# Performance work log

Hardware: AMD Instinct MI355X
Metric: run time of the kernel (lower is better)

## Reference

```python
import jax, jax.numpy as jnp
import numpy as np

WS = 8
NUM_HEADS = 8
BLUR_STRENGTH = 1.0
EPS = 1e-5


def setup_inputs() -> dict:
    key = jax.random.key(0)
    ks = jax.random.split(key, 8)
    B, C, H, W = 8, 256, 128, 128
    FF = 1024
    inp = {
        'x': jax.random.normal(ks[0], (B, C, H, W), jnp.float32),
        'blur_map': jax.random.uniform(ks[1], (B, 1, H // 4, W // 4), jnp.float32),
        'qkv_w': jax.random.normal(ks[2], (C, 3 * C), jnp.float32) * 0.02,
        'qkv_b': jnp.zeros((3 * C,), jnp.float32),
        'proj_w': jax.random.normal(ks[3], (C, C), jnp.float32) * 0.02,
        'proj_b': jnp.zeros((C,), jnp.float32),
        'ff1_w': jax.random.normal(ks[4], (C, FF), jnp.float32) * 0.02,
        'ff1_b': jnp.zeros((FF,), jnp.float32),
        'ff2_w': jax.random.normal(ks[5], (FF, C), jnp.float32) * 0.02,
        'ff2_b': jnp.zeros((C,), jnp.float32),
        'n1_g': jnp.ones((C,), jnp.float32),
        'n1_b': jnp.zeros((C,), jnp.float32),
        'n2_g': jnp.ones((C,), jnp.float32),
        'n2_b': jnp.zeros((C,), jnp.float32),
    }
    return inp


def _layer_norm(y, g, b):
    mu = jnp.mean(y, axis=-1, keepdims=True)
    var = jnp.mean(jnp.square(y - mu), axis=-1, keepdims=True)
    return (y - mu) * jax.lax.rsqrt(var + EPS) * g + b


def reference(x, blur_map, qkv_w, qkv_b, proj_w, proj_b, ff1_w, ff1_b, ff2_w, ff2_b, n1_g, n1_b, n2_g, n2_b):
    B, C, H, W = x.shape
    ws = WS
    h = NUM_HEADS
    hd = C // h
    T = ws * ws
    scale = C ** (-0.5)  # note: full dim, matching the torch module

    # window partition -> [nw, T, C]
    xw = x.reshape(B, C, H // ws, ws, W // ws, ws)
    xw = xw.transpose(0, 2, 4, 3, 5, 1).reshape(-1, T, C)
    nw = xw.shape[0]

    qkv = (xw @ qkv_w + qkv_b).reshape(nw, T, 3, h, hd).transpose(2, 0, 3, 1, 4)
    q, k, v = qkv[0], qkv[1], qkv[2]  # [nw, h, T, hd]

    attn = jnp.einsum('whid,whjd->whij', q, k) * scale

    # blur modulation along the key axis
    blur_down = jax.image.resize(blur_map, (B, 1, H, W), 'bilinear')
    blur_w = blur_down.reshape(B, 1, H // ws, ws, W // ws, ws)
    blur_w = blur_w.transpose(0, 2, 4, 3, 5, 1).reshape(nw, T)
    attn = attn * (1.0 + BLUR_STRENGTH * blur_w)[:, None, None, :]

    attn = jax.nn.softmax(attn, axis=-1)
    out = jnp.einsum('whij,whjd->whid', attn, v)
    out = out.transpose(0, 2, 1, 3).reshape(nw, T, C)
    out = out @ proj_w + proj_b

    x1 = xw + _layer_norm(out, n1_g, n1_b)
    ff = jnp.maximum(x1 @ ff1_w + ff1_b, 0.0) @ ff2_w + ff2_b
    x2 = x1 + _layer_norm(ff, n2_g, n2_b)

    # window reverse -> [B, C, H, W]
    x2 = x2.reshape(B, H // ws, W // ws, ws, ws, C)
    return x2.transpose(0, 5, 1, 3, 2, 4).reshape(B, C, H, W)
```

## Files before the change

kernel.cpp:

```cpp
#include <hip/hip_runtime.h>
#include <hip/hip_bf16.h>
#include <cstdint>

typedef _Float16 half8 __attribute__((ext_vector_type(8)));
typedef _Float16 half4 __attribute__((ext_vector_type(4)));
typedef float f32x4 __attribute__((ext_vector_type(4)));

__device__ __forceinline__ void gload_lds16(const _Float16* g, _Float16* l) {
  __builtin_amdgcn_global_load_lds(
      (const __attribute__((address_space(1))) void*)g,
      (__attribute__((address_space(3))) void*)l, 16, 0, 0);
}

#define KSWZ(r) ((((r) >> 1) & 3) << 3)

__global__ __launch_bounds__(256) void wtrans(const float* __restrict__ W,
                                              _Float16* __restrict__ WT, int K, int N) {
  int idx = blockIdx.x * 256 + threadIdx.x;
  if (idx >= K * N) return;
  int k = idx / N, n = idx - k * N;
  WT[(size_t)n * K + k] = (_Float16)W[idx];
}

__global__ __launch_bounds__(256) void blur_prep(const float* __restrict__ bm,
                                                 float* __restrict__ bw) {
  int idx = blockIdx.x * 256 + threadIdx.x;
  int wi = idx >> 6, t = idx & 63;
  int b = wi >> 8, wid = wi & 255;
  int hw = wid >> 4, ww = wid & 15;
  int hh = hw * 8 + (t >> 3), www = ww * 8 + (t & 7);
  float yf = (hh + 0.5f) * 0.25f - 0.5f;
  float xf = (www + 0.5f) * 0.25f - 0.5f;
  float yfl = floorf(yf), xfl = floorf(xf);
  float fy = yf - yfl, fx = xf - xfl;
  int y0 = (int)yfl, x0 = (int)xfl;
  int y1 = y0 + 1, x1 = x0 + 1;
  if (y0 < 0) y0 = 0; if (x0 < 0) x0 = 0;
  if (y1 > 31) y1 = 31; if (x1 > 31) x1 = 31;
  const float* p = bm + (size_t)b * 1024;
  float v00 = p[y0 * 32 + x0], v01 = p[y0 * 32 + x1];
  float v10 = p[y1 * 32 + x0], v11 = p[y1 * 32 + x1];
  float v0 = v00 + fx * (v01 - v00);
  float v1 = v10 + fx * (v11 - v10);
  bw[idx] = v0 + fy * (v1 - v0);
}

__global__ __launch_bounds__(256) void gather_x(const float* __restrict__ x,
                                                _Float16* __restrict__ xw) {
  const int c0 = blockIdx.x << 6;
  const int hh = blockIdx.y;
  const int b  = blockIdx.z;
  __shared__ float tile[64][133];
  const int tid = threadIdx.x;
  {
    const int cl = tid >> 7, p = tid & 127;
    const float* xp = x + ((size_t)(b * 256 + c0) * 128 + hh) * 128 + p;
#pragma unroll
    for (int i = 0; i < 32; ++i) {
      int c = i * 2 + cl;
      tile[c][p] = xp[(size_t)c * 16384];
    }
  }
  __syncthreads();
  const int w = tid >> 6, lane = tid & 63;
  const int hw = hh >> 3, ts = hh & 7;
#pragma unroll
  for (int i = 0; i < 32; ++i) {
    int pp = i * 4 + w;
    int row = ((b * 256 + hw * 16 + (pp >> 3)) << 6) + ts * 8 + (pp & 7);
    xw[(size_t)row * 256 + c0 + lane] = (_Float16)tile[lane][pp];
  }
}

__global__ __launch_bounds__(256) void scatter_out(const _Float16* __restrict__ x2,
                                                   float* __restrict__ out) {
  const int c0 = blockIdx.x << 6;
  const int hh = blockIdx.y;
  const int b  = blockIdx.z;
  __shared__ float tile[64][133];
  const int tid = threadIdx.x;
  const int w = tid >> 6, lane = tid & 63;
  const int hw = hh >> 3, ts = hh & 7;
#pragma unroll
  for (int i = 0; i < 32; ++i) {
    int pp = i * 4 + w;
    int row = ((b * 256 + hw * 16 + (pp >> 3)) << 6) + ts * 8 + (pp & 7);
    tile[lane][pp] = (float)x2[(size_t)row * 256 + c0 + lane];
  }
  __syncthreads();
  const int cl = tid >> 7, p = tid & 127;
  float* op = out + ((size_t)(b * 256 + c0) * 128 + hh) * 128 + p;
#pragma unroll
  for (int i = 0; i < 32; ++i) {
    int c = i * 2 + cl;
    op[(size_t)c * 16384] = tile[c][p];
  }
}

template<int RELU>
__global__ __launch_bounds__(256) void gemm_f16(const _Float16* __restrict__ A,
    const _Float16* __restrict__ BT, const float* __restrict__ bias,
    _Float16* __restrict__ C, int M, int N, int K) {
  __shared__ _Float16 As[2][128 * 32];
  __shared__ _Float16 Bs[2][128 * 32];
  const int tid = threadIdx.x;
  const int gx = gridDim.x;
  int flat = blockIdx.y * gx + blockIdx.x;
  int nwg = gx * gridDim.y;
  int nb = (nwg & 7) ? flat : ((flat & 7) * (nwg >> 3) + (flat >> 3));
  const int m0 = (nb / gx) << 7;
  const int n0 = (nb % gx) << 7;
  const int w = tid >> 6, lane = tid & 63;
  const int wr = (w >> 1) << 6, wc = (w & 1) << 6;
  const int lr = lane & 15, lg = lane >> 4;
  f32x4 acc[4][4] = {};
  const int sr = tid >> 2, skk = ((tid & 3) << 3) ^ KSWZ(tid >> 2);
  const _Float16* Ag = A + (size_t)(m0 + sr) * K + skk;
  const _Float16* Bg = BT + (size_t)(n0 + sr) * K + skk;
  const size_t halfstep = (size_t)64 * K;
#define GSTAGE(bufi, k0) do { \
    gload_lds16(Ag + (k0),            &As[bufi][(size_t)tid * 8]); \
    gload_lds16(Ag + (k0) + halfstep, &As[bufi][(size_t)(256 + tid) * 8]); \
    gload_lds16(Bg + (k0),            &Bs[bufi][(size_t)tid * 8]); \
    gload_lds16(Bg + (k0) + halfstep, &Bs[bufi][(size_t)(256 + tid) * 8]); \
  } while (0)
  GSTAGE(0, 0);
  __syncthreads();
  int cur = 0;
  for (int k0 = 0; k0 < K; k0 += 32) {
    if (k0 + 32 < K) GSTAGE(cur ^ 1, k0 + 32);
    half8 af[4], bf[4];
#pragma unroll
    for (int t = 0; t < 4; ++t) {
      int rowA = wr + t * 16 + lr;
      af[t] = *(const half8*)&As[cur][rowA * 32 + ((lg * 8) ^ KSWZ(rowA))];
    }
#pragma unroll
    for (int t = 0; t < 4; ++t) {
      int rowB = wc + t * 16 + lr;
      bf[t] = *(const half8*)&Bs[cur][rowB * 32 + ((lg * 8) ^ KSWZ(rowB))];
    }
#pragma unroll
    for (int i = 0; i < 4; ++i)
#pragma unroll
      for (int j = 0; j < 4; ++j)
        acc[i][j] = __builtin_amdgcn_mfma_f32_16x16x32_f16(af[i], bf[j], acc[i][j], 0, 0, 0);
    __syncthreads();
    cur ^= 1;
  }
#undef GSTAGE
  float bv[4];
#pragma unroll
  for (int j = 0; j < 4; ++j) bv[j] = bias[n0 + wc + j * 16 + lr];
#pragma unroll
  for (int i = 0; i < 4; ++i) {
#pragma unroll
    for (int j = 0; j < 4; ++j) {
      int row = m0 + wr + i * 16 + lg * 4;
      int col = n0 + wc + j * 16 + lr;
      _Float16* cp = C + (size_t)row * N + col;
#pragma unroll
      for (int rr = 0; rr < 4; ++rr) {
        float v = acc[i][j][rr] + bv[j];
        if (RELU) v = fmaxf(v, 0.0f);
        cp[(size_t)rr * N] = (_Float16)v;
      }
    }
  }
}

#define ATT_SWZ(row, col) (((row) << 6) + ((col) ^ (((row) & 7) << 3)))
__global__ __launch_bounds__(256, 3) void attn_mfma(const _Float16* __restrict__ qkv,
    const float* __restrict__ bw, _Float16* __restrict__ o) {
  const int wdw = blockIdx.x;
  const int w = threadIdx.x >> 6;
  const int lane = threadIdx.x & 63;
  const int lr = lane & 15, lg = lane >> 4;
  __shared__ _Float16 lds_p[4][64 * 64];
  __shared__ _Float16 lds_v[4][32 * 64];
  _Float16* Pb = lds_p[w];
  _Float16* Vt = lds_v[w];
  const size_t base = (size_t)wdw * 49152;
  f32x4 blv[4];
#pragma unroll
  for (int jt = 0; jt < 4; ++jt) {
    f32x4 bv = *(const f32x4*)&bw[wdw * 64 + jt * 16 + lg * 4];
    blv[jt] = bv * 0.0625f + 0.0625f;
  }
  const f32x4 zero4 = {0.f, 0.f, 0.f, 0.f};
#pragma unroll
  for (int hi = 0; hi < 2; ++hi) {
    const int h = w + hi * 4;
    const size_t qo = base + (size_t)h * 32;
    const _Float16* kp = qkv + qo + 256 + (size_t)lr * 768 + lg * 8;
    const _Float16* qp = qkv + qo +       (size_t)lr * 768 + lg * 8;
    half8 ak[4], bq[4];
#pragma unroll
    for (int t = 0; t < 4; ++t) {
      ak[t] = *(const half8*)(kp + (size_t)t * 16 * 768);
      bq[t] = *(const half8*)(qp + (size_t)t * 16 * 768);
    }
    const _Float16* vp = qkv + qo + 512 + (size_t)lane * 768;
#pragma unroll
    for (int e = 0; e < 4; ++e) {
      half8 vv = *(const half8*)(vp + e * 8);
#pragma unroll
      for (int d = 0; d < 8; ++d) Vt[ATT_SWZ(e * 8 + d, lane)] = vv[d];
    }
    f32x4 cst[4][4];
#pragma unroll
    for (int jt = 0; jt < 4; ++jt)
#pragma unroll
      for (int it = 0; it < 4; ++it)
        cst[jt][it] = __builtin_amdgcn_mfma_f32_16x16x32_f16(ak[jt], bq[it], zero4, 0, 0, 0);
#pragma unroll
    for (int it = 0; it < 4; ++it) {
      float m = -1e30f;
#pragma unroll
      for (int jt = 0; jt < 4; ++jt) {
        cst[jt][it] *= blv[jt];
        m = fmaxf(m, fmaxf(fmaxf(cst[jt][it][0], cst[jt][it][1]),
                           fmaxf(cst[jt][it][2], cst[jt][it][3])));
      }
      m = fmaxf(m, __shfl_xor(m, 16, 64));
      m = fmaxf(m, __shfl_xor(m, 32, 64));
      float s = 0.f;
#pragma unroll
      for (int jt = 0; jt < 4; ++jt)
#pragma unroll
        for (int r = 0; r < 4; ++r) {
          float e = __expf(cst[jt][it][r] - m);
          cst[jt][it][r] = e;
          s += e;
        }
      s += __shfl_xor(s, 16, 64);
      s += __shfl_xor(s, 32, 64);
      float inv = 1.0f / s;
#pragma unroll
      for (int jt = 0; jt < 4; ++jt) {
        half4 pv;
#pragma unroll
        for (int r = 0; r < 4; ++r) pv[r] = (_Float16)(cst[jt][it][r] * inv);
        *(half4*)&Pb[ATT_SWZ(it * 16 + lr, jt * 16 + lg * 4)] = pv;
      }
    }
    f32x4 co[4][2] = {};
#pragma unroll
    for (int ks = 0; ks < 2; ++ks) {
      half8 bv2[2], pa[4];
#pragma unroll
      for (int dt = 0; dt < 2; ++dt)
        bv2[dt] = *(const half8*)&Vt[ATT_SWZ(dt * 16 + lr, ks * 32 + lg * 8)];
#pragma unroll
      for (int it = 0; it < 4; ++it)
        pa[it] = *(const half8*)&Pb[ATT_SWZ(it * 16 + lr, ks * 32 + lg * 8)];
#pragma unroll
      for (int it = 0; it < 4; ++it)
#pragma unroll
        for (int dt = 0; dt < 2; ++dt)
          co[it][dt] = __builtin_amdgcn_mfma_f32_16x16x32_f16(pa[it], bv2[dt], co[it][dt], 0, 0, 0);
    }
#pragma unroll
    for (int it = 0; it < 4; ++it)
#pragma unroll
      for (int dt = 0; dt < 2; ++dt)
#pragma unroll
        for (int r = 0; r < 4; ++r) {
          int row = it * 16 + lg * 4 + r;
          o[((size_t)wdw * 64 + row) * 256 + h * 32 + dt * 16 + lr] =
              (_Float16)co[it][dt][r];
        }
  }
}

__global__ __launch_bounds__(256) void ln_add(const _Float16* __restrict__ inp,
    const _Float16* __restrict__ res, const float* __restrict__ gg,
    const float* __restrict__ bb, _Float16* __restrict__ out) {
  const int w = threadIdx.x >> 6, lane = threadIdx.x & 63;
  const size_t row = (size_t)blockIdx.x * 4 + w;
  half4 v = ((const half4*)(inp + row * 256))[lane];
  float f0 = (float)v[0], f1 = (float)v[1], f2 = (float)v[2], f3 = (float)v[3];
  float s = f0 + f1 + f2 + f3;
  float s2 = f0*f0 + f1*f1 + f2*f2 + f3*f3;
#pragma unroll
  for (int m = 1; m < 64; m <<= 1) {
    s  += __shfl_xor(s, m, 64);
    s2 += __shfl_xor(s2, m, 64);
  }
  float mu = s * 0.00390625f;
  float var = s2 * 0.00390625f - mu * mu;
  float rs = rsqrtf(var + 1e-5f);
  f32x4 gv = *(const f32x4*)(gg + lane * 4);
  f32x4 bv = *(const f32x4*)(bb + lane * 4);
  half4 rv = ((const half4*)(res + row * 256))[lane];
  half4 ov;
  ov[0] = (_Float16)((f0 - mu) * rs * gv[0] + bv[0] + (float)rv[0]);
  ov[1] = (_Float16)((f1 - mu) * rs * gv[1] + bv[1] + (float)rv[1]);
  ov[2] = (_Float16)((f2 - mu) * rs * gv[2] + bv[2] + (float)rv[2]);
  ov[3] = (_Float16)((f3 - mu) * rs * gv[3] + bv[3] + (float)rv[3]);
  ((half4*)(out + row * 256))[lane] = ov;
}

__global__ __launch_bounds__(256) void sentinel(float* out, int n) {
  int i = blockIdx.x * 256 + threadIdx.x;
  if (i < n) out[i] = 12345.0f;
}

extern "C" void kernel_launch(void* const* d_in, const int* in_sizes, int n_in,
                              void* d_out, int out_size, void* d_ws, size_t ws_size,
                              hipStream_t stream) {
  const float* x      = (const float*)d_in[0];
  const float* blurm  = (const float*)d_in[1];
  const float* qkv_w  = (const float*)d_in[2];
  const float* qkv_b  = (const float*)d_in[3];
  const float* proj_w = (const float*)d_in[4];
  const float* proj_b = (const float*)d_in[5];
  const float* ff1_w  = (const float*)d_in[6];
  const float* ff1_b  = (const float*)d_in[7];
  const float* ff2_w  = (const float*)d_in[8];
  const float* ff2_b  = (const float*)d_in[9];
  const float* n1_g   = (const float*)d_in[10];
  const float* n1_b   = (const float*)d_in[11];
  const float* n2_g   = (const float*)d_in[12];
  const float* n2_b   = (const float*)d_in[13];
  float* out = (float*)d_out;

  char* ws = (char*)d_ws;
  constexpr size_t OFF_RA  = 0;
  constexpr size_t OFF_XW  = 201326592ull;
  constexpr size_t OFF_AO  = OFF_XW + 67108864ull;
  constexpr size_t OFF_RC  = OFF_AO + 67108864ull;
  constexpr size_t OFF_X1  = OFF_RC + 67108864ull;
  constexpr size_t OFF_QW  = OFF_X1 + 67108864ull;
  constexpr size_t OFF_PW  = OFF_QW + 393216ull;
  constexpr size_t OFF_F1W = OFF_PW + 131072ull;
  constexpr size_t OFF_F2W = OFF_F1W + 524288ull;
  constexpr size_t OFF_BL  = OFF_F2W + 524288ull;
  constexpr size_t NEED    = OFF_BL + 524288ull;
  if (ws_size < NEED) {
    sentinel<<<(out_size + 255) / 256, 256, 0, stream>>>(out, out_size);
    return;
  }
  _Float16* RA   = (_Float16*)(ws + OFF_RA);
  _Float16* xw_h = (_Float16*)(ws + OFF_XW);
  _Float16* ao   = (_Float16*)(ws + OFF_AO);
  _Float16* rc   = (_Float16*)(ws + OFF_RC);
  _Float16* x1h  = (_Float16*)(ws + OFF_X1);
  _Float16* qwT  = (_Float16*)(ws + OFF_QW);
  _Float16* pwT  = (_Float16*)(ws + OFF_PW);
  _Float16* f1wT = (_Float16*)(ws + OFF_F1W);
  _Float16* f2wT = (_Float16*)(ws + OFF_F2W);
  float* blurw   = (float*)(ws + OFF_BL);

  wtrans<<<768, 256, 0, stream>>>(qkv_w, qwT, 256, 768);
  wtrans<<<256, 256, 0, stream>>>(proj_w, pwT, 256, 256);
  wtrans<<<1024, 256, 0, stream>>>(ff1_w, f1wT, 256, 1024);
  wtrans<<<1024, 256, 0, stream>>>(ff2_w, f2wT, 1024, 256);
  blur_prep<<<512, 256, 0, stream>>>(blurm, blurw);
  gather_x<<<dim3(4, 128, 8), 256, 0, stream>>>(x, xw_h);

  gemm_f16<0><<<dim3(6, 1024), 256, 0, stream>>>(xw_h, qwT, qkv_b, RA, 131072, 768, 256);
  attn_mfma<<<2048, 256, 0, stream>>>(RA, blurw, ao);
  gemm_f16<0><<<dim3(2, 1024), 256, 0, stream>>>(ao, pwT, proj_b, rc, 131072, 256, 256);
  ln_add<<<32768, 256, 0, stream>>>(rc, xw_h, n1_g, n1_b, x1h);
  for (int ch = 0; ch < 2; ++ch) {
    const size_t off = (size_t)ch * 65536 * 256;
    gemm_f16<1><<<dim3(8, 512), 256, 0, stream>>>(x1h + off, f1wT, ff1_b,
                                                  RA, 65536, 1024, 256);
    gemm_f16<0><<<dim3(2, 512), 256, 0, stream>>>(RA, f2wT, ff2_b,
                                                  rc + off, 65536, 256, 1024);
  }
  ln_add<<<32768, 256, 0, stream>>>(rc, x1h, n2_g, n2_b, xw_h);
  scatter_out<<<dim3(4, 128, 8), 256, 0, stream>>>(xw_h, out);
}
```

Baseline: 618.3 us.

## Triple-buffer GEMM LDS tiles with explicit vmcnt waits and single barrier

```diff
diff --git a/kernel.cpp b/kernel.cpp
--- a/kernel.cpp
+++ b/kernel.cpp
@@ -101,8 +101,8 @@
 __global__ __launch_bounds__(256) void gemm_f16(const _Float16* __restrict__ A,
     const _Float16* __restrict__ BT, const float* __restrict__ bias,
     _Float16* __restrict__ C, int M, int N, int K) {
-  __shared__ _Float16 As[2][128 * 32];
-  __shared__ _Float16 Bs[2][128 * 32];
+  __shared__ _Float16 As[3][128 * 32];
+  __shared__ _Float16 Bs[3][128 * 32];
   const int tid = threadIdx.x;
   const int gx = gridDim.x;
   int flat = blockIdx.y * gx + blockIdx.x;
@@ -124,29 +124,38 @@
     gload_lds16(Bg + (k0),            &Bs[bufi][(size_t)tid * 8]); \
     gload_lds16(Bg + (k0) + halfstep, &Bs[bufi][(size_t)(256 + tid) * 8]); \
   } while (0)
+  const int nsteps = K >> 5;
   GSTAGE(0, 0);
-  __syncthreads();
+  GSTAGE(1, 32);
   int cur = 0;
-  for (int k0 = 0; k0 < K; k0 += 32) {
-    if (k0 + 32 < K) GSTAGE(cur ^ 1, k0 + 32);
+  for (int t = 0; t < nsteps; ++t) {
+    if (t + 1 < nsteps) {
+      asm volatile("s_waitcnt vmcnt(4)" ::: "memory");
+    } else {
+      asm volatile("s_waitcnt vmcnt(0)" ::: "memory");
+    }
+    __builtin_amdgcn_s_barrier();
     half8 af[4], bf[4];
 #pragma unroll
-    for (int t = 0; t < 4; ++t) {
-      int rowA = wr + t * 16 + lr;
-      af[t] = *(const half8*)&As[cur][rowA * 32 + ((lg * 8) ^ KSWZ(rowA))];
-    }
-#pragma unroll
-    for (int t = 0; t < 4; ++t) {
-      int rowB = wc + t * 16 + lr;
-      bf[t] = *(const half8*)&Bs[cur][rowB * 32 + ((lg * 8) ^ KSWZ(rowB))];
+    for (int tt = 0; tt < 4; ++tt) {
+      int rowA = wr + tt * 16 + lr;
+      af[tt] = *(const half8*)&As[cur][rowA * 32 + ((lg * 8) ^ KSWZ(rowA))];
+    }
+#pragma unroll
+    for (int tt = 0; tt < 4; ++tt) {
+      int rowB = wc + tt * 16 + lr;
+      bf[tt] = *(const half8*)&Bs[cur][rowB * 32 + ((lg * 8) ^ KSWZ(rowB))];
     }
 #pragma unroll
     for (int i = 0; i < 4; ++i)
 #pragma unroll
       for (int j = 0; j < 4; ++j)
         acc[i][j] = __builtin_amdgcn_mfma_f32_16x16x32_f16(af[i], bf[j], acc[i][j], 0, 0, 0);
-    __syncthreads();
-    cur ^= 1;
+    if (t + 2 < nsteps) {
+      int nxt = cur + 2; if (nxt >= 3) nxt -= 3;
+      GSTAGE(nxt, (t + 2) * 32);
+    }
+    cur = (cur == 2) ? 0 : cur + 1;
   }
 #undef GSTAGE
   float bv[4];
```

After: 602.2 us. -2.6%, faster.

## Load GEMM B operand directly from global to registers; unchunk FFN GEMMs

Applied to the files above, without the earlier changes.

```diff
diff --git a/kernel.cpp b/kernel.cpp
--- a/kernel.cpp
+++ b/kernel.cpp
@@ -102,7 +102,6 @@
     const _Float16* __restrict__ BT, const float* __restrict__ bias,
     _Float16* __restrict__ C, int M, int N, int K) {
   __shared__ _Float16 As[2][128 * 32];
-  __shared__ _Float16 Bs[2][128 * 32];
   const int tid = threadIdx.x;
   const int gx = gridDim.x;
   int flat = blockIdx.y * gx + blockIdx.x;
@@ -116,29 +115,27 @@
   f32x4 acc[4][4] = {};
   const int sr = tid >> 2, skk = ((tid & 3) << 3) ^ KSWZ(tid >> 2);
   const _Float16* Ag = A + (size_t)(m0 + sr) * K + skk;
-  const _Float16* Bg = BT + (size_t)(n0 + sr) * K + skk;
+  const _Float16* Bg0 = BT + (size_t)(n0 + wc + lr) * K + lg * 8;
   const size_t halfstep = (size_t)64 * K;
-#define GSTAGE(bufi, k0) do { \
+  const size_t bstep = (size_t)16 * K;
+#define ASTAGE(bufi, k0) do { \
     gload_lds16(Ag + (k0),            &As[bufi][(size_t)tid * 8]); \
     gload_lds16(Ag + (k0) + halfstep, &As[bufi][(size_t)(256 + tid) * 8]); \
-    gload_lds16(Bg + (k0),            &Bs[bufi][(size_t)tid * 8]); \
-    gload_lds16(Bg + (k0) + halfstep, &Bs[bufi][(size_t)(256 + tid) * 8]); \
   } while (0)
-  GSTAGE(0, 0);
+  ASTAGE(0, 0);
   __syncthreads();
   int cur = 0;
   for (int k0 = 0; k0 < K; k0 += 32) {
-    if (k0 + 32 < K) GSTAGE(cur ^ 1, k0 + 32);
-    half8 af[4], bf[4];
+    if (k0 + 32 < K) ASTAGE(cur ^ 1, k0 + 32);
+    half8 bf[4];
+#pragma unroll
+    for (int t = 0; t < 4; ++t)
+      bf[t] = *(const half8*)(Bg0 + (size_t)t * bstep + k0);
+    half8 af[4];
 #pragma unroll
     for (int t = 0; t < 4; ++t) {
       int rowA = wr + t * 16 + lr;
       af[t] = *(const half8*)&As[cur][rowA * 32 + ((lg * 8) ^ KSWZ(rowA))];
-    }
-#pragma unroll
-    for (int t = 0; t < 4; ++t) {
-      int rowB = wc + t * 16 + lr;
-      bf[t] = *(const half8*)&Bs[cur][rowB * 32 + ((lg * 8) ^ KSWZ(rowB))];
     }
 #pragma unroll
     for (int i = 0; i < 4; ++i)
@@ -148,7 +145,7 @@
     __syncthreads();
     cur ^= 1;
   }
-#undef GSTAGE
+#undef ASTAGE
   float bv[4];
 #pragma unroll
   for (int j = 0; j < 4; ++j) bv[j] = bias[n0 + wc + j * 16 + lr];
@@ -342,6 +339,7 @@
     return;
   }
   _Float16* RA   = (_Float16*)(ws + OFF_RA);
+  _Float16* F    = (_Float16*)(ws + OFF_RA);
   _Float16* xw_h = (_Float16*)(ws + OFF_XW);
   _Float16* ao   = (_Float16*)(ws + OFF_AO);
   _Float16* rc   = (_Float16*)(ws + OFF_RC);
@@ -363,13 +361,8 @@
   attn_mfma<<<2048, 256, 0, stream>>>(RA, blurw, ao);
   gemm_f16<0><<<dim3(2, 1024), 256, 0, stream>>>(ao, pwT, proj_b, rc, 131072, 256, 256);
   ln_add<<<32768, 256, 0, stream>>>(rc, xw_h, n1_g, n1_b, x1h);
-  for (int ch = 0; ch < 2; ++ch) {
-    const size_t off = (size_t)ch * 65536 * 256;
-    gemm_f16<1><<<dim3(8, 512), 256, 0, stream>>>(x1h + off, f1wT, ff1_b,
-                                                  RA, 65536, 1024, 256);
-    gemm_f16<0><<<dim3(2, 512), 256, 0, stream>>>(RA, f2wT, ff2_b,
-                                                  rc + off, 65536, 256, 1024);
-  }
+  gemm_f16<1><<<dim3(8, 1024), 256, 0, stream>>>(x1h, f1wT, ff1_b, F, 131072, 1024, 256);
+  gemm_f16<0><<<dim3(2, 1024), 256, 0, stream>>>(F, f2wT, ff2_b, rc, 131072, 256, 1024);
   ln_add<<<32768, 256, 0, stream>>>(rc, x1h, n2_g, n2_b, xw_h);
   scatter_out<<<dim3(4, 128, 8), 256, 0, stream>>>(xw_h, out);
 }
```

Measured after the change: 788.8 us. 1.28x slower.
